# Performance work log

Hardware: AMD Instinct MI355X
Metric: run time of the kernel (lower is better)

The kernel has to match this reference:

```python
import jax, jax.numpy as jnp
import numpy as np

EPS = 1e-6
GATE_SCALE = 1.0
Z = 0.0 + 0.1j  # config.z_real + i*config.z_imag


def setup_inputs() -> dict:
    key = jax.random.key(0)
    ks = jax.random.split(key, 8)
    B, S, H, D = 2, 1024, 16, 2048
    x = jax.random.normal(ks[0], (B, S, D), dtype=jnp.float32)
    attention_weights = jax.random.uniform(ks[1], (B, H, S, S), dtype=jnp.float32)
    # projection weights: init per module (std=1e-4; he_diag bias = 1, others 0)
    Wd = jax.random.normal(ks[2], (D, D), dtype=jnp.float32) * 1e-4
    bd = jnp.ones((D,), dtype=jnp.float32)
    Wsup = jax.random.normal(ks[3], (D, D), dtype=jnp.float32) * 1e-4
    bsup = jnp.zeros((D,), dtype=jnp.float32)
    Wsub = jax.random.normal(ks[4], (D, D), dtype=jnp.float32) * 1e-4
    bsub = jnp.zeros((D,), dtype=jnp.float32)
    gW = jax.random.normal(ks[5], (1, 2), dtype=jnp.float32) * 1e-4
    gb = jnp.ones((1,), dtype=jnp.float32)
    return dict(x=x, attention_weights=attention_weights, Wd=Wd, bd=bd,
                Wsup=Wsup, bsup=bsup, Wsub=Wsub, bsub=bsub, gW=gW, gb=gb)


def reference(x, attention_weights, Wd, bd, Wsup, bsup, Wsub, bsub, gW, gb):
    # tridiagonal projections, reduced over feature dim -> [B, S] scalars per position
    he_diag = (jnp.einsum('bsd,ed->bse', x, Wd) + bd).mean(axis=-1)            # [B, S]
    h0_super = (jnp.einsum('bsd,ed->bse', x[:, :-1], Wsup) + bsup).mean(-1)    # [B, S-1] (dead in simple path)
    h0_sub = (jnp.einsum('bsd,ed->bse', x[:, 1:], Wsub) + bsub).mean(-1)       # [B, S-1] (dead in simple path)
    del h0_super, h0_sub  # BKCoreFunction unavailable -> _simple_green_function ignores off-diagonals
    # simple Green's function: G_ii = 1 / (he_diag - z + EPS)
    G = 1.0 / (he_diag.astype(jnp.complex64) - jnp.complex64(Z) + EPS)         # [B, S] complex64
    # scattering gate: sigmoid(Linear([Re G, Im G]) * gate_scale)
    feats = jnp.stack([jnp.real(G), jnp.imag(G)], axis=-1)                     # [B, S, 2]
    gate = jax.nn.sigmoid((feats @ gW.T + gb)[..., 0] * GATE_SCALE)            # [B, S]
    gated = attention_weights * gate[:, None, :, None]                         # [B, H, S, S]
    return gated / (gated.sum(axis=-1, keepdims=True) + EPS)
```

## Files before the change

### kernel.cpp

```cpp
#include <hip/hip_runtime.h>

#define EPSF 1e-6f
#define DD 2048
#define SS 1024
#define BB 2
#define HH 16

typedef float fx4 __attribute__((ext_vector_type(4)));


__global__ __launch_bounds__(256) void k_colsum(const float* __restrict__ Wd,
                                                float* __restrict__ wsum) {
    int dchunk = blockIdx.x & 7;
    int echunk = blockIdx.x >> 3;
    int d = dchunk * 256 + threadIdx.x;
    const float* p = Wd + (size_t)(echunk * 64) * DD + d;
    float acc = 0.f;
#pragma unroll 8
    for (int e = 0; e < 64; ++e) acc += p[(size_t)e * DD];
    atomicAdd(wsum + d, acc);
}

__global__ __launch_bounds__(256) void k_gate(const float* __restrict__ x,
                                              const float* __restrict__ wsum,
                                              const float* __restrict__ bd,
                                              const float* __restrict__ gW,
                                              const float* __restrict__ gb,
                                              float* __restrict__ gate) {
    int p = blockIdx.x;
    int t = threadIdx.x;
    const fx4* xr = (const fx4*)(x + (size_t)p * DD);
    const fx4* wr = (const fx4*)wsum;
    const fx4* br = (const fx4*)bd;
    float accd = 0.f, accb = 0.f;
#pragma unroll
    for (int k = 0; k < 2; ++k) {
        fx4 xv = xr[t + k * 256];
        fx4 wv = wr[t + k * 256];
        fx4 bv = br[t + k * 256];
        accd += xv.x * wv.x + xv.y * wv.y + xv.z * wv.z + xv.w * wv.w;
        accb += bv.x + bv.y + bv.z + bv.w;
    }
    __shared__ float redd[4], redb[4];
#pragma unroll
    for (int off = 32; off > 0; off >>= 1) {
        accd += __shfl_down(accd, off);
        accb += __shfl_down(accb, off);
    }
    if ((t & 63) == 0) { redd[t >> 6] = accd; redb[t >> 6] = accb; }
    __syncthreads();
    if (t == 0) {
        float he = (redd[0] + redd[1] + redd[2] + redd[3] +
                    redb[0] + redb[1] + redb[2] + redb[3]) * (1.f / DD);
        float a = he + EPSF;
        float den = a * a + 0.01f;
        float lin = (a * gW[0] + 0.1f * gW[1]) / den + gb[0];
        gate[p] = 1.f / (1.f + expf(-lin));
    }
}

__global__ __launch_bounds__(256) void k_norm(const float* __restrict__ aw,
                                              const float* __restrict__ gate,
                                              float* __restrict__ out) {
    int row = blockIdx.x * 4 + (threadIdx.x >> 6);
    int lane = threadIdx.x & 63;
    size_t base = (size_t)row * SS;
    const fx4* r = (const fx4*)(aw + base);
    fx4 v[4];
    float acc = 0.f;
#pragma unroll
    for (int k = 0; k < 4; ++k) {
        v[k] = __builtin_nontemporal_load(r + lane + k * 64);
        acc += v[k].x + v[k].y + v[k].z + v[k].w;
    }
#pragma unroll
    for (int off = 1; off < 64; off <<= 1) acc += __shfl_xor(acc, off);
    int s = row & (SS - 1);
    int b = row >> 14;
    float g = gate[(b << 10) + s];
    float scale = g / (g * acc + EPSF);
    fx4* o = (fx4*)(out + base);
#pragma unroll
    for (int k = 0; k < 4; ++k) {
        fx4 w = v[k] * scale;
        __builtin_nontemporal_store(w, o + lane + k * 64);
    }
}

extern "C" void kernel_launch(void* const* d_in, const int* in_sizes, int n_in,
                              void* d_out, int out_size, void* d_ws, size_t ws_size,
                              hipStream_t stream) {
    const float* x  = (const float*)d_in[0];
    const float* aw = (const float*)d_in[1];
    const float* Wd = (const float*)d_in[2];
    const float* bd = (const float*)d_in[3];
    const float* gW = (const float*)d_in[8];
    const float* gb = (const float*)d_in[9];
    float* out = (float*)d_out;
    float* ws = (float*)d_ws;
    float* wsum = ws;
    float* gate = ws + 2560;

    (void)hipMemsetAsync(wsum, 0, DD * sizeof(float), stream);
    k_colsum<<<256, 256, 0, stream>>>(Wd, wsum);
    k_gate<<<BB * SS, 256, 0, stream>>>(x, wsum, bd, gW, gb, gate);
    k_norm<<<8192, 256, 0, stream>>>(aw, gate, out);
}
```

Baseline: 279.3 us.

## Fuse gate computation into normalization kernel and fold bias sum into colsum

Removes the separate gate kernel. Each normalization block now handles four heads of one (batch, position) row and computes the x·colsum dot product and sigmoid gate itself. The bias sum moves into the column-sum kernel as one extra scalar atomically accumulated in the workspace. This saves a launch and the gate round-trip through memory, but each x row is now read and reduced once per head group, four times in total, adding redundant traffic and compute next to the attention-weight stream.

```diff
diff --git a/kernel.cpp b/kernel.cpp
--- a/kernel.cpp
+++ b/kernel.cpp
@@ -10,7 +10,8 @@
 
 
 __global__ __launch_bounds__(256) void k_colsum(const float* __restrict__ Wd,
-                                                float* __restrict__ wsum) {
+                                                const float* __restrict__ bd,
+                                                float* __restrict__ ws) {
     int dchunk = blockIdx.x & 7;
     int echunk = blockIdx.x >> 3;
     int d = dchunk * 256 + threadIdx.x;
@@ -18,72 +19,70 @@
     float acc = 0.f;
 #pragma unroll 8
     for (int e = 0; e < 64; ++e) acc += p[(size_t)e * DD];
-    atomicAdd(wsum + d, acc);
+    atomicAdd(ws + d, acc);
+    if (echunk == 0) {
+        float accb = bd[d];
+#pragma unroll
+        for (int off = 32; off > 0; off >>= 1) accb += __shfl_down(accb, off);
+        __shared__ float rb[4];
+        if ((threadIdx.x & 63) == 0) rb[threadIdx.x >> 6] = accb;
+        __syncthreads();
+        if (threadIdx.x == 0) atomicAdd(ws + DD, rb[0] + rb[1] + rb[2] + rb[3]);
+    }
 }
 
-__global__ __launch_bounds__(256) void k_gate(const float* __restrict__ x,
-                                              const float* __restrict__ wsum,
-                                              const float* __restrict__ bd,
+__global__ __launch_bounds__(256) void k_norm(const float* __restrict__ aw,
+                                              const float* __restrict__ x,
+                                              const float* __restrict__ ws,
                                               const float* __restrict__ gW,
                                               const float* __restrict__ gb,
-                                              float* __restrict__ gate) {
-    int p = blockIdx.x;
+                                              float* __restrict__ out) {
     int t = threadIdx.x;
-    const fx4* xr = (const fx4*)(x + (size_t)p * DD);
-    const fx4* wr = (const fx4*)wsum;
-    const fx4* br = (const fx4*)bd;
-    float accd = 0.f, accb = 0.f;
+    int w = t >> 6, lane = t & 63;
+    int bid = blockIdx.x;
+    int s = bid & (SS - 1);
+    int hg = (bid >> 10) & 3;
+    int b = bid >> 12;
+    int h = hg * 4 + w;
+    size_t rowbase = ((size_t)((b * HH + h) * SS + s)) * SS;
+    const fx4* r = (const fx4*)(aw + rowbase);
+    fx4 v[4];
+#pragma unroll
+    for (int k = 0; k < 4; ++k)
+        v[k] = __builtin_nontemporal_load(r + lane + k * 64);
+
+    const fx4* xr = (const fx4*)(x + ((size_t)(b * SS + s)) * DD);
+    const fx4* wr = (const fx4*)ws;
+    float accd = 0.f;
 #pragma unroll
     for (int k = 0; k < 2; ++k) {
         fx4 xv = xr[t + k * 256];
         fx4 wv = wr[t + k * 256];
-        fx4 bv = br[t + k * 256];
         accd += xv.x * wv.x + xv.y * wv.y + xv.z * wv.z + xv.w * wv.w;
-        accb += bv.x + bv.y + bv.z + bv.w;
     }
-    __shared__ float redd[4], redb[4];
 #pragma unroll
-    for (int off = 32; off > 0; off >>= 1) {
-        accd += __shfl_down(accd, off);
-        accb += __shfl_down(accb, off);
-    }
-    if ((t & 63) == 0) { redd[t >> 6] = accd; redb[t >> 6] = accb; }
+    for (int off = 32; off > 0; off >>= 1) accd += __shfl_down(accd, off);
+    __shared__ float redd[4];
+    if (lane == 0) redd[w] = accd;
     __syncthreads();
-    if (t == 0) {
-        float he = (redd[0] + redd[1] + redd[2] + redd[3] +
-                    redb[0] + redb[1] + redb[2] + redb[3]) * (1.f / DD);
-        float a = he + EPSF;
-        float den = a * a + 0.01f;
-        float lin = (a * gW[0] + 0.1f * gW[1]) / den + gb[0];
-        gate[p] = 1.f / (1.f + expf(-lin));
-    }
-}
+    float he = (redd[0] + redd[1] + redd[2] + redd[3] + ws[DD]) * (1.f / DD);
+    float a = he + EPSF;
+    float den = a * a + 0.01f;
+    float lin = (a * gW[0] + 0.1f * gW[1]) / den + gb[0];
+    float g = 1.f / (1.f + expf(-lin));
 
-__global__ __launch_bounds__(256) void k_norm(const float* __restrict__ aw,
-                                              const float* __restrict__ gate,
-                                              float* __restrict__ out) {
-    int row = blockIdx.x * 4 + (threadIdx.x >> 6);
-    int lane = threadIdx.x & 63;
-    size_t base = (size_t)row * SS;
-    const fx4* r = (const fx4*)(aw + base);
-    fx4 v[4];
     float acc = 0.f;
 #pragma unroll
-    for (int k = 0; k < 4; ++k) {
-        v[k] = __builtin_nontemporal_load(r + lane + k * 64);
+    for (int k = 0; k < 4; ++k)
         acc += v[k].x + v[k].y + v[k].z + v[k].w;
-    }
 #pragma unroll
     for (int off = 1; off < 64; off <<= 1) acc += __shfl_xor(acc, off);
-    int s = row & (SS - 1);
-    int b = row >> 14;
-    float g = gate[(b << 10) + s];
     float scale = g / (g * acc + EPSF);
-    fx4* o = (fx4*)(out + base);
+    fx4* o = (fx4*)(out + rowbase);
 #pragma unroll
     for (int k = 0; k < 4; ++k) {
-        fx4 w = v[k] * scale;
-        __builtin_nontemporal_store(w, o + lane + k * 64);
+        fx4 wv = v[k] * scale;
+        __builtin_nontemporal_store(wv, o + lane + k * 64);
     }
 }
 
@@ -98,11 +97,8 @@
     const float* gb = (const float*)d_in[9];
     float* out = (float*)d_out;
     float* ws = (float*)d_ws;
-    float* wsum = ws;
-    float* gate = ws + 2560;
 
-    (void)hipMemsetAsync(wsum, 0, DD * sizeof(float), stream);
-    k_colsum<<<256, 256, 0, stream>>>(Wd, wsum);
-    k_gate<<<BB * SS, 256, 0, stream>>>(x, wsum, bd, gW, gb, gate);
-    k_norm<<<8192, 256, 0, stream>>>(aw, gate, out);
+    (void)hipMemsetAsync(ws, 0, (DD + 1) * sizeof(float), stream);
+    k_colsum<<<256, 256, 0, stream>>>(Wd, bd, ws);
+    k_norm<<<BB * HH * SS / 4, 256, 0, stream>>>(aw, x, ws, gW, gb, out);
 }
```

Result: no change. 283.2 us (+1.4%).
